# Optimization experiments

Measured on AMD Instinct MI355X. Metric: run time of the kernel, lower is better.

The kernel has to match this reference:

```python
import jax, jax.numpy as jnp
import numpy as np

B, S, D = 64, 512, 768
H1, H2, NC = 256, 128, 1
THR = 0.1  # attention_threshold in original forward


def setup_inputs() -> dict:
    key = jax.random.key(0)
    k0, k1, k2, k3 = jax.random.split(key, 4)
    # scale hidden states so H @ H^T logits are in a reasonable softmax range
    hidden_states = jax.random.normal(k0, (B, S, D), jnp.float32) * 0.05
    attention_mask = jnp.ones((B, S), jnp.int32)
    W1 = jax.random.normal(k1, (D, H1), jnp.float32) * (1.0 / np.sqrt(D))
    b1 = jnp.zeros((H1,), jnp.float32)
    W2 = jax.random.normal(k2, (H1, H2), jnp.float32) * (1.0 / np.sqrt(H1))
    b2 = jnp.zeros((H2,), jnp.float32)
    Wc = jax.random.normal(k3, (H2, NC), jnp.float32) * (1.0 / np.sqrt(H2))
    bc = jnp.zeros((NC,), jnp.float32)
    return dict(hidden_states=hidden_states, attention_mask=attention_mask,
                W1=W1, b1=b1, W2=W2, b2=b2, Wc=Wc, bc=bc)


def _gcn_adj(att):
    # thresholded sparse graph, expressed as masked dense adjacency [B,S,S]
    A = jnp.where(att > THR, att, 0.0)
    # PyG add_remaining_self_loops: keep existing self-loop weight, else fill 1.0
    diag = jnp.diagonal(att, axis1=-2, axis2=-1)            # [B,S]
    diag = jnp.where(diag > THR, diag, 1.0)
    i = jnp.arange(att.shape[-1])
    A = A.at[:, i, i].set(diag)
    # gcn_norm: deg over targets (columns), D^{-1/2} A D^{-1/2}
    deg = A.sum(axis=-2)                                     # [B,S]
    dis = jnp.where(deg > 0, jax.lax.rsqrt(deg), 0.0)
    return dis[:, :, None] * A * dis[:, None, :]


def _gcn_layer(Ahat, x, W, b):
    xw = x @ W                                               # linear first (no bias)
    # out[target j] = sum_source i  Ahat[i,j] * xw[i]
    return jnp.einsum('bij,bih->bjh', Ahat, xw) + b


def reference(hidden_states, attention_mask, W1, b1, W2, b2, Wc, bc):
    att = jax.nn.softmax(
        jnp.einsum('bsd,btd->bst', hidden_states, hidden_states), axis=-1)
    Ahat = _gcn_adj(att)                                     # [B,S,S]
    x = jax.nn.relu(_gcn_layer(Ahat, hidden_states, W1, b1))  # dropout inactive (eval)
    x = _gcn_layer(Ahat, x, W2, b2)                          # [B,S,H2]
    m = attention_mask.astype(x.dtype)                       # masked mean over valid tokens
    emb = (x * m[:, :, None]).sum(axis=1) / m.sum(axis=1, keepdims=True)
    return jax.nn.sigmoid(emb @ Wc + bc)                     # [B,1]
```

## Files before the change

kernel.cpp:

```cpp
#include <hip/hip_runtime.h>
#include <hip/hip_bf16.h>
#include <math.h>

constexpr int B = 64, S = 512, D = 768, H1 = 256, H2 = 128;
constexpr float THR = 0.1f;

typedef short bf16x8 __attribute__((ext_vector_type(8)));
typedef float f32x4 __attribute__((ext_vector_type(4)));
typedef unsigned int uint_t;
typedef const __attribute__((address_space(1))) unsigned int* gptr_t;
typedef __attribute__((address_space(3))) unsigned int* lptr_t;

__device__ __forceinline__ unsigned short f2bf(float f) {
    unsigned int u = __builtin_bit_cast(unsigned int, f);
    unsigned int r = (u + 0x7FFFu + ((u >> 16) & 1u)) >> 16;
    return (unsigned short)r;
}
__device__ __forceinline__ float bf2f(unsigned short b) {
    return __builtin_bit_cast(float, (unsigned int)b << 16);
}
__device__ __forceinline__ unsigned char f2fp8(float f) {
    uint_t u = __builtin_bit_cast(uint_t, f);
    u += 0x7FFFFu + ((u >> 20) & 1u);
    return (unsigned char)((((u >> 23) - 120u) << 3) | ((u >> 20) & 7u));
}
__device__ __forceinline__ float fp82f(unsigned char q) {
    uint_t e = (q >> 3) & 0xFu, m = q & 7u;
    if (e == 0) return (float)m * 0.001953125f;
    return __builtin_bit_cast(float, ((e + 120u) << 23) | (m << 20));
}
__device__ __forceinline__ void gl2lds16(const void* g, void* l) {
    __builtin_amdgcn_global_load_lds((gptr_t)g, (lptr_t)l, 16, 0, 0);
}

__global__ __launch_bounds__(256) void k_cast(const float* __restrict__ in,
                                              short* __restrict__ out,
                                              const float* __restrict__ W1,
                                              short* __restrict__ W1T,
                                              const float* __restrict__ W2,
                                              short* __restrict__ W2T,
                                              float* __restrict__ zbuf) {
    const int id = blockIdx.x * 256 + threadIdx.x;
    if (id < 18432) ((float4*)zbuf)[id] = make_float4(0.f, 0.f, 0.f, 0.f);
    if (id < 196608) {
        const int n = id / D, k = id - n * D;
        W1T[id] = (short)f2bf(W1[(size_t)k * H1 + n]);
    } else if (id < 229376) {
        const int i2 = id - 196608;
        const int n = i2 / H1, k = i2 - n * H1;
        W2T[i2] = (short)f2bf(W2[(size_t)k * H2 + n]);
    }
    for (int i = id; i < 3145728; i += 524288) {
        float4 a = ((const float4*)in)[i * 2];
        float4 b = ((const float4*)in)[i * 2 + 1];
        uint4 o;
        o.x = (uint_t)f2bf(a.x) | ((uint_t)f2bf(a.y) << 16);
        o.y = (uint_t)f2bf(a.z) | ((uint_t)f2bf(a.w) << 16);
        o.z = (uint_t)f2bf(b.x) | ((uint_t)f2bf(b.y) << 16);
        o.w = (uint_t)f2bf(b.z) | ((uint_t)f2bf(b.w) << 16);
        ((uint4*)out)[i] = o;
    }
}

__global__ __launch_bounds__(256) void k_logits(const short* __restrict__ Hb_,
                                                unsigned char* __restrict__ L8,
                                                float* __restrict__ rsum) {
    const int orig = blockIdx.x;
    const int wg = (orig & 7) * 128 + (orig >> 3);
    const int bz = wg >> 4;
    const int bi = (wg >> 2) & 3, bj = wg & 3;
    const short* Ab = Hb_ + (size_t)bz * S * D;
    unsigned char* Lb = L8 + (size_t)bz * S * S;
    float* rs = rsum + bz * S;
    const int M0 = bi * 128, N0 = bj * 128;

    __shared__ __align__(16) short As[8192];
    __shared__ __align__(16) short Bs[8192];

    const int tid = threadIdx.x, lane = tid & 63, wid = tid >> 6;
    const int wm = (wid & 1) * 64, wn = (wid >> 1) * 64;
    const int r_in = lane >> 3, kc = lane & 7;
    const int kswz = ((kc ^ r_in) << 3);

    f32x4 zero = {0.f, 0.f, 0.f, 0.f};
    f32x4 acc[4][4];
    #pragma unroll
    for (int mi = 0; mi < 4; ++mi)
        #pragma unroll
        for (int nj = 0; nj < 4; ++nj) acc[mi][nj] = zero;

    for (int t = 0; t < 12; ++t) {
        const int kt = t * 64;
        #pragma unroll
        for (int q = 0; q < 4; ++q) {
            const int ch = wid * 4 + q;
            gl2lds16(Ab + (size_t)(M0 + ch * 8 + r_in) * D + kt + kswz, &As[ch * 512]);
        }
        #pragma unroll
        for (int q = 0; q < 4; ++q) {
            const int ch = wid * 4 + q;
            gl2lds16(Ab + (size_t)(N0 + ch * 8 + r_in) * D + kt + kswz, &Bs[ch * 512]);
        }
        __syncthreads();
        #pragma unroll
        for (int kk = 0; kk < 2; ++kk) {
            bf16x8 af[4], bfr[4];
            const int g0 = kk * 4 + (lane >> 4);
            #pragma unroll
            for (int mi = 0; mi < 4; ++mi) {
                const int row = wm + mi * 16 + (lane & 15);
                af[mi] = *(const bf16x8*)&As[row * 64 + ((g0 ^ (row & 7)) << 3)];
            }
            #pragma unroll
            for (int nj = 0; nj < 4; ++nj) {
                const int row = wn + nj * 16 + (lane & 15);
                bfr[nj] = *(const bf16x8*)&Bs[row * 64 + ((g0 ^ (row & 7)) << 3)];
            }
            #pragma unroll
            for (int mi = 0; mi < 4; ++mi)
                #pragma unroll
                for (int nj = 0; nj < 4; ++nj)
                    acc[mi][nj] = __builtin_amdgcn_mfma_f32_16x16x32_bf16(
                        af[mi], bfr[nj], acc[mi][nj], 0, 0, 0);
        }
        __syncthreads();
    }

    #pragma unroll
    for (int mi = 0; mi < 4; ++mi)
        #pragma unroll
        for (int nj = 0; nj < 4; ++nj) {
            f32x4 v = acc[mi][nj];
            acc[mi][nj][0] = __expf(v[0]);
            acc[mi][nj][1] = __expf(v[1]);
            acc[mi][nj][2] = __expf(v[2]);
            acc[mi][nj][3] = __expf(v[3]);
        }

    #pragma unroll
    for (int mi = 0; mi < 4; ++mi) {
        const int mb = wm + mi * 16 + (lane >> 4) * 4;
        #pragma unroll
        for (int nj = 0; nj < 4; ++nj) {
            const int n = wn + nj * 16 + (lane & 15);
            f32x4 v = acc[mi][nj];
            uchar4 o;
            o.x = f2fp8(v[0]); o.y = f2fp8(v[1]);
            o.z = f2fp8(v[2]); o.w = f2fp8(v[3]);
            *(uchar4*)&Lb[(size_t)(N0 + n) * S + M0 + mb] = o;
        }
    }

    #pragma unroll
    for (int mi = 0; mi < 4; ++mi)
        #pragma unroll
        for (int r = 0; r < 4; ++r) {
            float s = acc[mi][0][r] + acc[mi][1][r] + acc[mi][2][r] + acc[mi][3][r];
            s += __shfl_xor(s, 1); s += __shfl_xor(s, 2);
            s += __shfl_xor(s, 4); s += __shfl_xor(s, 8);
            if ((lane & 15) == 0)
                atomicAdd(&rs[M0 + wm + mi * 16 + (lane >> 4) * 4 + r], s);
        }
}

__global__ __launch_bounds__(256) void k_prep_gemm(
    const unsigned char* __restrict__ L8, const float* __restrict__ rsum,
    const int* __restrict__ mask, float* __restrict__ dis,
    float* __restrict__ wacc, uint_t* __restrict__ ents, uint_t* __restrict__ cnts,
    const short* __restrict__ W1T, const short* __restrict__ Hb,
    short* __restrict__ xw1) {
    __shared__ __align__(16) short As[128 * 64];
    __shared__ __align__(16) short Bs[64 * 64];

    const int blk = blockIdx.x;
    const int r9 = blk % 9;
    const int tid = threadIdx.x, lane = tid & 63, wid = tid >> 6;

    if (r9 != 8) {
        const int p = (blk / 9) * 8 + r9;
        const int j = p * 4 + (tid >> 6);
        const int b = j >> 9, jl = j & (S - 1);
        const size_t base = (size_t)b * S * S + (size_t)jl * S + lane * 8;
        const uint2 r = *(const uint2*)(L8 + base);
        const int i0 = lane * 8;
        const float4 sa = *(const float4*)&rsum[b * S + i0];
        const float4 sb = *(const float4*)&rsum[b * S + i0 + 4];
        const float rsv[8] = {sa.x, sa.y, sa.z, sa.w, sb.x, sb.y, sb.z, sb.w};
        float a[8];
        float deg = 0.f;
        #pragma unroll
        for (int e = 0; e < 8; ++e) {
            const unsigned char q = (e < 4) ? (unsigned char)(r.x >> (e * 8))
                                            : (unsigned char)(r.y >> ((e - 4) * 8));
            float att = fp82f(q) / rsv[e];
            if (i0 + e == jl) a[e] = (att > THR) ? att : 1.0f;
            else              a[e] = (att > THR) ? att : 0.0f;
            deg += a[e];
        }
        #pragma unroll
        for (int off = 1; off < 64; off <<= 1) deg += __shfl_xor(deg, off);
        const float d = (deg > 0.f) ? rsqrtf(deg) : 0.f;
        const float cv = d * (float)mask[j];
        if (lane == 0) dis[j] = d;
        #pragma unroll
        for (int e = 0; e < 8; ++e)
            if (a[e] != 0.f) atomicAdd(&wacc[b * S + i0 + e], cv * a[e]);

        unsigned long long bl[8];
        #pragma unroll
        for (int e = 0; e < 8; ++e) bl[e] = __ballot(a[e] != 0.f);
        const unsigned long long lt = (lane == 0) ? 0ull : (~0ull >> (64 - lane));
        int pre = 0, tot = 0;
        #pragma unroll
        for (int e = 0; e < 8; ++e) {
            pre += __popcll(bl[e] & lt);
            tot += __popcll(bl[e]);
        }
        uint_t* rowents = ents + (size_t)j * S;
        int own = 0;
        #pragma unroll
        for (int e = 0; e < 8; ++e) {
            if (a[e] != 0.f) {
                rowents[pre + own] = ((uint_t)(i0 + e) << 16) | (uint_t)f2bf(a[e]);
                ++own;
            }
        }
        if (lane == 0) cnts[j] = (uint_t)tot;
        return;
    }

    const int orig = blk / 9;
    const int wg = (orig & 7) * 128 + (orig >> 3);
    const int bx = wg & 1, by = wg >> 1;
    const int M0 = bx * 128, N0 = by * 64;

    const int wm = (wid & 1) * 64, wn = (wid >> 1) * 32;
    const int r_in = lane >> 3, kc = lane & 7;
    const int kswz = ((kc ^ r_in) << 3);

    f32x4 zero = {0.f, 0.f, 0.f, 0.f};
    f32x4 acc[4][2];
    #pragma unroll
    for (int mi = 0; mi < 4; ++mi) {
        acc[mi][0] = zero; acc[mi][1] = zero;
    }

    for (int t = 0; t < 12; ++t) {
        const int kt = t << 6;
        #pragma unroll
        for (int q = 0; q < 4; ++q) {
            const int ch = wid * 4 + q;
            gl2lds16(W1T + (size_t)(M0 + ch * 8 + r_in) * D + kt + kswz, &As[ch * 512]);
        }
        #pragma unroll
        for (int q = 0; q < 2; ++q) {
            const int ch = wid * 2 + q;
            gl2lds16(Hb + (size_t)(N0 + ch * 8 + r_in) * D + kt + kswz, &Bs[ch * 512]);
        }
        __syncthreads();
        #pragma unroll
        for (int kk = 0; kk < 2; ++kk) {
            bf16x8 af[4], bfr[2];
            const int g0 = kk * 4 + (lane >> 4);
            #pragma unroll
            for (int mi = 0; mi < 4; ++mi) {
                const int row = wm + mi * 16 + (lane & 15);
                af[mi] = *(const bf16x8*)&As[row * 64 + ((g0 ^ (row & 7)) << 3)];
            }
            #pragma unroll
            for (int nj = 0; nj < 2; ++nj) {
                const int row = wn + nj * 16 + (lane & 15);
                bfr[nj] = *(const bf16x8*)&Bs[row * 64 + ((g0 ^ (row & 7)) << 3)];
            }
            #pragma unroll
            for (int mi = 0; mi < 4; ++mi)
                #pragma unroll
                for (int nj = 0; nj < 2; ++nj)
                    acc[mi][nj] = __builtin_amdgcn_mfma_f32_16x16x32_bf16(
                        af[mi], bfr[nj], acc[mi][nj], 0, 0, 0);
        }
        __syncthreads();
    }

    #pragma unroll
    for (int mi = 0; mi < 4; ++mi) {
        const int m = M0 + wm + mi * 16 + (lane >> 4) * 4;
        #pragma unroll
        for (int nj = 0; nj < 2; ++nj) {
            const int n = N0 + wn + nj * 16 + (lane & 15);
            f32x4 v = acc[mi][nj];
            ushort4 o = make_ushort4(f2bf(v[0]), f2bf(v[1]), f2bf(v[2]), f2bf(v[3]));
            *(ushort4*)&xw1[(size_t)n * H1 + m] = o;
        }
    }
}

__global__ __launch_bounds__(256) void k_agg(const uint_t* __restrict__ ents,
                                             const uint_t* __restrict__ cnts,
                                             const float* __restrict__ dis,
                                             const short* __restrict__ xw1,
                                             const float* __restrict__ b1,
                                             short* __restrict__ y1) {
    const int tid = threadIdx.x;
    const int h = tid;
    const float bias = b1[h];
    __shared__ uint_t sents[S];
    for (int jj = 0; jj < 8; ++jj) {
        const int j = blockIdx.x * 8 + jj;
        const int b = j >> 9;
        const int cnt = (int)cnts[j];
        for (int k = tid; k < cnt; k += 256) sents[k] = ents[(size_t)j * S + k];
        __syncthreads();
        float acc = 0.f;
        for (int k = 0; k < cnt; ++k) {
            const uint_t p = sents[k];
            const int i = (int)(p >> 16);
            const float val = bf2f((unsigned short)(p & 0xFFFFu)) * dis[b * S + i];
            acc += val * bf2f((unsigned short)xw1[(size_t)(b * S + i) * H1 + h]);
        }
        const float o = fmaxf(dis[j] * acc + bias, 0.f);
        y1[(size_t)j * H1 + h] = (short)f2bf(o);
        __syncthreads();
    }
}

__global__ __launch_bounds__(256) void k_gemm_emb(
    const short* __restrict__ W2T, const short* __restrict__ y1,
    const float* __restrict__ wacc, const float* __restrict__ dis,
    float* __restrict__ embp) {
    const int orig = blockIdx.x;
    const int wg = (orig & 7) * 64 + (orig >> 3);
    const int N0 = wg * 64;

    __shared__ __align__(16) short As[128 * 64];
    __shared__ __align__(16) short Bs[64 * 64];

    const int tid = threadIdx.x, lane = tid & 63, wid = tid >> 6;
    const int wm = (wid & 1) * 64, wn = (wid >> 1) * 32;
    const int r_in = lane >> 3, kc = lane & 7;
    const int kswz = ((kc ^ r_in) << 3);

    f32x4 zero = {0.f, 0.f, 0.f, 0.f};
    f32x4 acc[4][2];
    #pragma unroll
    for (int mi = 0; mi < 4; ++mi) {
        acc[mi][0] = zero; acc[mi][1] = zero;
    }

    for (int t = 0; t < 4; ++t) {
        const int kt = t << 6;
        #pragma unroll
        for (int q = 0; q < 4; ++q) {
            const int ch = wid * 4 + q;
            gl2lds16(W2T + (size_t)(ch * 8 + r_in) * H1 + kt + kswz, &As[ch * 512]);
        }
        #pragma unroll
        for (int q = 0; q < 2; ++q) {
            const int ch = wid * 2 + q;
            gl2lds16(y1 + (size_t)(N0 + ch * 8 + r_in) * H1 + kt + kswz, &Bs[ch * 512]);
        }
        __syncthreads();
        #pragma unroll
        for (int kk = 0; kk < 2; ++kk) {
            bf16x8 af[4], bfr[2];
            const int g0 = kk * 4 + (lane >> 4);
            #pragma unroll
            for (int mi = 0; mi < 4; ++mi) {
                const int row = wm + mi * 16 + (lane & 15);
                af[mi] = *(const bf16x8*)&As[row * 64 + ((g0 ^ (row & 7)) << 3)];
            }
            #pragma unroll
            for (int nj = 0; nj < 2; ++nj) {
                const int row = wn + nj * 16 + (lane & 15);
                bfr[nj] = *(const bf16x8*)&Bs[row * 64 + ((g0 ^ (row & 7)) << 3)];
            }
            #pragma unroll
            for (int mi = 0; mi < 4; ++mi)
                #pragma unroll
                for (int nj = 0; nj < 2; ++nj)
                    acc[mi][nj] = __builtin_amdgcn_mfma_f32_16x16x32_bf16(
                        af[mi], bfr[nj], acc[mi][nj], 0, 0, 0);
        }
        __syncthreads();
    }

    const int bb = N0 >> 9;
    float wv[2];
    #pragma unroll
    for (int nj = 0; nj < 2; ++nj) {
        const int gn = N0 + wn + nj * 16 + (lane & 15);
        wv[nj] = wacc[gn] * dis[gn];
    }
    #pragma unroll
    for (int mi = 0; mi < 4; ++mi)
        #pragma unroll
        for (int r = 0; r < 4; ++r) {
            float s = acc[mi][0][r] * wv[0] + acc[mi][1][r] * wv[1];
            s += __shfl_xor(s, 1); s += __shfl_xor(s, 2);
            s += __shfl_xor(s, 4); s += __shfl_xor(s, 8);
            if ((lane & 15) == 0) {
                const int h = wm + mi * 16 + (lane >> 4) * 4 + r;
                atomicAdd(&embp[bb * H2 + h], s);
            }
        }
}

__global__ __launch_bounds__(128) void k_final(const float* __restrict__ emb,
                                               const int* __restrict__ mask,
                                               const float* __restrict__ b2,
                                               const float* __restrict__ Wc,
                                               const float* __restrict__ bc,
                                               float* __restrict__ out) {
    const int b = blockIdx.x;
    const int h = threadIdx.x;
    const int* mb = mask + b * S;

    float msum = 0.f;
    for (int i = h; i < S; i += 128) msum += (float)mb[i];
    #pragma unroll
    for (int off = 1; off < 64; off <<= 1) msum += __shfl_xor(msum, off);
    __shared__ float redm[2], redv[2];
    if ((h & 63) == 0) redm[h >> 6] = msum;
    __syncthreads();
    msum = redm[0] + redm[1];

    const float e = b2[h] + emb[b * H2 + h] / msum;
    float val = e * Wc[h];
    #pragma unroll
    for (int off = 1; off < 64; off <<= 1) val += __shfl_xor(val, off);
    if ((h & 63) == 0) redv[h >> 6] = val;
    __syncthreads();
    if (h == 0) {
        float z = redv[0] + redv[1] + bc[0];
        out[b] = 1.f / (1.f + expf(-z));
    }
}

extern "C" void kernel_launch(void* const* d_in, const int* in_sizes, int n_in,
                              void* d_out, int out_size, void* d_ws, size_t ws_size,
                              hipStream_t stream) {
    const float* H    = (const float*)d_in[0];
    const int*   mask = (const int*)d_in[1];
    const float* W1   = (const float*)d_in[2];
    const float* b1   = (const float*)d_in[3];
    const float* W2   = (const float*)d_in[4];
    const float* b2   = (const float*)d_in[5];
    const float* Wc   = (const float*)d_in[6];
    const float* bc   = (const float*)d_in[7];
    float* out = (float*)d_out;

    const int NTOK = B * S;

    char* wsb = (char*)d_ws;
    short* Hb    = (short*)(wsb);
    short* y1    = (short*)(wsb);
    unsigned char* Lbuf = (unsigned char*)(wsb + 50331648);
    short* xw1   = (short*)(wsb + 83886080);
    float* rsum  = (float*)(wsb + 109051904);
    float* wacc  = rsum + NTOK;
    float* emb   = wacc + NTOK;
    float* dis   = emb + 8192;
    short* W1T   = (short*)(dis + NTOK);
    short* W2T   = W1T + 196608;
    uint_t* ents = (uint_t*)(wsb + 134217728);
    uint_t* cnts = (uint_t*)(wsb + 201326592);

    k_cast<<<2048, 256, 0, stream>>>(H, Hb, W1, W1T, W2, W2T, rsum);

    k_logits<<<1024, 256, 0, stream>>>(Hb, Lbuf, rsum);

    k_prep_gemm<<<9216, 256, 0, stream>>>(Lbuf, rsum, mask, dis, wacc, ents, cnts,
                                          W1T, Hb, xw1);

    k_agg<<<4096, 256, 0, stream>>>(ents, cnts, dis, xw1, b1, y1);

    k_gemm_emb<<<512, 256, 0, stream>>>(W2T, y1, wacc, dis, emb);

    k_final<<<B, 128, 0, stream>>>(emb, mask, b2, Wc, bc, out);
}
```

Measured before the change: 142.7 us.

## Fuse fp32-to-bf16 cast of hidden states into logits GEMM tile loads

The separate pass that converted the full hidden-state tensor to bf16 is removed. The logits kernel now reads fp32 directly, converts it in registers and stores into LDS. Diagonal tiles also write the bf16 copy to global memory for later kernels, and they reuse the A tile as the B operand. This removes a full read and write of the hidden states and one launch. In exchange the logits kernel does twice the global load bytes through plain synchronous loads instead of async global-to-LDS loads, which exposes more load latency.

Measured after the change: 151.5 us. +6.2%, slower.

```diff
diff --git a/kernel.cpp b/kernel.cpp
--- a/kernel.cpp
+++ b/kernel.cpp
@@ -32,10 +32,16 @@
 __device__ __forceinline__ void gl2lds16(const void* g, void* l) {
     __builtin_amdgcn_global_load_lds((gptr_t)g, (lptr_t)l, 16, 0, 0);
 }
-
-__global__ __launch_bounds__(256) void k_cast(const float* __restrict__ in,
-                                              short* __restrict__ out,
-                                              const float* __restrict__ W1,
+__device__ __forceinline__ uint4 pack8(const float4& a, const float4& b) {
+    uint4 o;
+    o.x = (uint_t)f2bf(a.x) | ((uint_t)f2bf(a.y) << 16);
+    o.y = (uint_t)f2bf(a.z) | ((uint_t)f2bf(a.w) << 16);
+    o.z = (uint_t)f2bf(b.x) | ((uint_t)f2bf(b.y) << 16);
+    o.w = (uint_t)f2bf(b.z) | ((uint_t)f2bf(b.w) << 16);
+    return o;
+}
+
+__global__ __launch_bounds__(256) void k_cast(const float* __restrict__ W1,
                                               short* __restrict__ W1T,
                                               const float* __restrict__ W2,
                                               short* __restrict__ W2T,
@@ -50,26 +56,19 @@
         const int n = i2 / H1, k = i2 - n * H1;
         W2T[i2] = (short)f2bf(W2[(size_t)k * H2 + n]);
     }
-    for (int i = id; i < 3145728; i += 524288) {
-        float4 a = ((const float4*)in)[i * 2];
-        float4 b = ((const float4*)in)[i * 2 + 1];
-        uint4 o;
-        o.x = (uint_t)f2bf(a.x) | ((uint_t)f2bf(a.y) << 16);
-        o.y = (uint_t)f2bf(a.z) | ((uint_t)f2bf(a.w) << 16);
-        o.z = (uint_t)f2bf(b.x) | ((uint_t)f2bf(b.y) << 16);
-        o.w = (uint_t)f2bf(b.z) | ((uint_t)f2bf(b.w) << 16);
-        ((uint4*)out)[i] = o;
-    }
-}
-
-__global__ __launch_bounds__(256) void k_logits(const short* __restrict__ Hb_,
+}
+
+__global__ __launch_bounds__(256) void k_logits(const float* __restrict__ H,
+                                                short* __restrict__ HbW,
                                                 unsigned char* __restrict__ L8,
                                                 float* __restrict__ rsum) {
     const int orig = blockIdx.x;
     const int wg = (orig & 7) * 128 + (orig >> 3);
     const int bz = wg >> 4;
     const int bi = (wg >> 2) & 3, bj = wg & 3;
-    const short* Ab = Hb_ + (size_t)bz * S * D;
+    const bool diag = (bi == bj);
+    const float* Hf = H + (size_t)bz * S * D;
+    short* Hw = HbW + (size_t)bz * S * D;
     unsigned char* Lb = L8 + (size_t)bz * S * S;
     float* rs = rsum + bz * S;
     const int M0 = bi * 128, N0 = bj * 128;
@@ -80,7 +79,6 @@
     const int tid = threadIdx.x, lane = tid & 63, wid = tid >> 6;
     const int wm = (wid & 1) * 64, wn = (wid >> 1) * 64;
     const int r_in = lane >> 3, kc = lane & 7;
-    const int kswz = ((kc ^ r_in) << 3);
 
     f32x4 zero = {0.f, 0.f, 0.f, 0.f};
     f32x4 acc[4][4];
@@ -89,17 +87,29 @@
         #pragma unroll
         for (int nj = 0; nj < 4; ++nj) acc[mi][nj] = zero;
 
+    const short* Bsrc = diag ? As : Bs;
+
     for (int t = 0; t < 12; ++t) {
-        const int kt = t * 64;
+        const int col = t * 64 + ((kc ^ r_in) << 3);
         #pragma unroll
         for (int q = 0; q < 4; ++q) {
             const int ch = wid * 4 + q;
-            gl2lds16(Ab + (size_t)(M0 + ch * 8 + r_in) * D + kt + kswz, &As[ch * 512]);
-        }
-        #pragma unroll
-        for (int q = 0; q < 4; ++q) {
-            const int ch = wid * 4 + q;
-            gl2lds16(Ab + (size_t)(N0 + ch * 8 + r_in) * D + kt + kswz, &Bs[ch * 512]);
+            const int row = M0 + ch * 8 + r_in;
+            const float4 a = *(const float4*)&Hf[(size_t)row * D + col];
+            const float4 b = *(const float4*)&Hf[(size_t)row * D + col + 4];
+            const uint4 o = pack8(a, b);
+            *(uint4*)&As[ch * 512 + lane * 8] = o;
+            if (diag) *(uint4*)&Hw[(size_t)row * D + col] = o;
+        }
+        if (!diag) {
+            #pragma unroll
+            for (int q = 0; q < 4; ++q) {
+                const int ch = wid * 4 + q;
+                const int row = N0 + ch * 8 + r_in;
+                const float4 a = *(const float4*)&Hf[(size_t)row * D + col];
+                const float4 b = *(const float4*)&Hf[(size_t)row * D + col + 4];
+                *(uint4*)&Bs[ch * 512 + lane * 8] = pack8(a, b);
+            }
         }
         __syncthreads();
         #pragma unroll
@@ -114,7 +124,7 @@
             #pragma unroll
             for (int nj = 0; nj < 4; ++nj) {
                 const int row = wn + nj * 16 + (lane & 15);
-                bfr[nj] = *(const bf16x8*)&Bs[row * 64 + ((g0 ^ (row & 7)) << 3)];
+                bfr[nj] = *(const bf16x8*)&Bsrc[row * 64 + ((g0 ^ (row & 7)) << 3)];
             }
             #pragma unroll
             for (int mi = 0; mi < 4; ++mi)
@@ -465,9 +475,9 @@
     uint_t* ents = (uint_t*)(wsb + 134217728);
     uint_t* cnts = (uint_t*)(wsb + 201326592);
 
-    k_cast<<<2048, 256, 0, stream>>>(H, Hb, W1, W1T, W2, W2T, rsum);
-
-    k_logits<<<1024, 256, 0, stream>>>(Hb, Lbuf, rsum);
+    k_cast<<<1024, 256, 0, stream>>>(W1, W1T, W2, W2T, rsum);
+
+    k_logits<<<1024, 256, 0, stream>>>(H, Hb, Lbuf, rsum);
 
     k_prep_gemm<<<9216, 256, 0, stream>>>(Lbuf, rsum, mask, dis, wacc, ents, cnts,
                                           W1T, Hb, xw1);
```

## Fuse sparse layer-1 aggregation into layer-2 GEMM with y1 kept in LDS

Applied to the files above, without the earlier changes.

Merges the sparse aggregation kernel into the second GEMM/embedding kernel: each 64-token block first computes its relu'd layer-1 outputs into padded shared memory, then feeds them directly as the B operand of the MFMA GEMM. It also changes aggregation from one token per 256-thread block to one token per wavefront, with each lane covering four features and edges broadcast by shuffle instead of LDS plus syncthreads. This drops the y1 global round-trip and a kernel launch, but the grid falls from 4096 to 512 blocks, so the irregular aggregation has less parallelism and may be bound by latency.

New measurement: 145.2 us. Within noise of the previous version (+1.7%).

```diff
diff --git a/kernel.cpp b/kernel.cpp
--- a/kernel.cpp
+++ b/kernel.cpp
@@ -295,47 +295,49 @@
     }
 }
 
-__global__ __launch_bounds__(256) void k_agg(const uint_t* __restrict__ ents,
-                                             const uint_t* __restrict__ cnts,
-                                             const float* __restrict__ dis,
-                                             const short* __restrict__ xw1,
-                                             const float* __restrict__ b1,
-                                             short* __restrict__ y1) {
-    const int tid = threadIdx.x;
-    const int h = tid;
-    const float bias = b1[h];
-    __shared__ uint_t sents[S];
-    for (int jj = 0; jj < 8; ++jj) {
-        const int j = blockIdx.x * 8 + jj;
-        const int b = j >> 9;
-        const int cnt = (int)cnts[j];
-        for (int k = tid; k < cnt; k += 256) sents[k] = ents[(size_t)j * S + k];
-        __syncthreads();
-        float acc = 0.f;
-        for (int k = 0; k < cnt; ++k) {
-            const uint_t p = sents[k];
-            const int i = (int)(p >> 16);
-            const float val = bf2f((unsigned short)(p & 0xFFFFu)) * dis[b * S + i];
-            acc += val * bf2f((unsigned short)xw1[(size_t)(b * S + i) * H1 + h]);
-        }
-        const float o = fmaxf(dis[j] * acc + bias, 0.f);
-        y1[(size_t)j * H1 + h] = (short)f2bf(o);
-        __syncthreads();
-    }
-}
-
-__global__ __launch_bounds__(256) void k_gemm_emb(
-    const short* __restrict__ W2T, const short* __restrict__ y1,
-    const float* __restrict__ wacc, const float* __restrict__ dis,
-    float* __restrict__ embp) {
+__global__ __launch_bounds__(256) void k_agg_emb(
+    const uint_t* __restrict__ ents, const uint_t* __restrict__ cnts,
+    const float* __restrict__ dis, const float* __restrict__ wacc,
+    const short* __restrict__ xw1, const float* __restrict__ b1,
+    const short* __restrict__ W2T, float* __restrict__ embp) {
+    constexpr int YP = 264;
+    __shared__ __align__(16) short y1s[64 * YP];
+    __shared__ __align__(16) short As[128 * 64];
+
     const int orig = blockIdx.x;
     const int wg = (orig & 7) * 64 + (orig >> 3);
     const int N0 = wg * 64;
-
-    __shared__ __align__(16) short As[128 * 64];
-    __shared__ __align__(16) short Bs[64 * 64];
-
+    const int b = N0 >> 9;
     const int tid = threadIdx.x, lane = tid & 63, wid = tid >> 6;
+
+    for (int u = 0; u < 16; ++u) {
+        const int jj = wid * 16 + u;
+        const int j = N0 + jj;
+        const int cnt = (int)cnts[j];
+        float acc0 = 0.f, acc1 = 0.f, acc2 = 0.f, acc3 = 0.f;
+        for (int k0 = 0; k0 < cnt; k0 += 64) {
+            uint_t my = 0;
+            if (k0 + lane < cnt) my = ents[(size_t)j * S + k0 + lane];
+            const int lim = (cnt - k0 < 64) ? (cnt - k0) : 64;
+            for (int k = 0; k < lim; ++k) {
+                const uint_t p = __shfl(my, k);
+                const int i = (int)(p >> 16);
+                const float val = bf2f((unsigned short)(p & 0xFFFFu)) * dis[b * S + i];
+                const short* xr = &xw1[(size_t)(b * S + i) * H1];
+                acc0 += val * bf2f((unsigned short)xr[lane]);
+                acc1 += val * bf2f((unsigned short)xr[lane + 64]);
+                acc2 += val * bf2f((unsigned short)xr[lane + 128]);
+                acc3 += val * bf2f((unsigned short)xr[lane + 192]);
+            }
+        }
+        const float dj = dis[j];
+        y1s[jj * YP + lane      ] = (short)f2bf(fmaxf(dj * acc0 + b1[lane      ], 0.f));
+        y1s[jj * YP + lane + 64 ] = (short)f2bf(fmaxf(dj * acc1 + b1[lane + 64 ], 0.f));
+        y1s[jj * YP + lane + 128] = (short)f2bf(fmaxf(dj * acc2 + b1[lane + 128], 0.f));
+        y1s[jj * YP + lane + 192] = (short)f2bf(fmaxf(dj * acc3 + b1[lane + 192], 0.f));
+    }
+    __syncthreads();
+
     const int wm = (wid & 1) * 64, wn = (wid >> 1) * 32;
     const int r_in = lane >> 3, kc = lane & 7;
     const int kswz = ((kc ^ r_in) << 3);
@@ -354,11 +356,6 @@
             const int ch = wid * 4 + q;
             gl2lds16(W2T + (size_t)(ch * 8 + r_in) * H1 + kt + kswz, &As[ch * 512]);
         }
-        #pragma unroll
-        for (int q = 0; q < 2; ++q) {
-            const int ch = wid * 2 + q;
-            gl2lds16(y1 + (size_t)(N0 + ch * 8 + r_in) * H1 + kt + kswz, &Bs[ch * 512]);
-        }
         __syncthreads();
         #pragma unroll
         for (int kk = 0; kk < 2; ++kk) {
@@ -371,8 +368,9 @@
             }
             #pragma unroll
             for (int nj = 0; nj < 2; ++nj) {
-                const int row = wn + nj * 16 + (lane & 15);
-                bfr[nj] = *(const bf16x8*)&Bs[row * 64 + ((g0 ^ (row & 7)) << 3)];
+                const int tok = wn + nj * 16 + (lane & 15);
+                const int col = kt + kk * 32 + (lane >> 4) * 8;
+                bfr[nj] = *(const bf16x8*)&y1s[tok * YP + col];
             }
             #pragma unroll
             for (int mi = 0; mi < 4; ++mi)
@@ -384,7 +382,6 @@
         __syncthreads();
     }
 
-    const int bb = N0 >> 9;
     float wv[2];
     #pragma unroll
     for (int nj = 0; nj < 2; ++nj) {
@@ -400,7 +397,7 @@
             s += __shfl_xor(s, 4); s += __shfl_xor(s, 8);
             if ((lane & 15) == 0) {
                 const int h = wm + mi * 16 + (lane >> 4) * 4 + r;
-                atomicAdd(&embp[bb * H2 + h], s);
+                atomicAdd(&embp[b * H2 + h], s);
             }
         }
 }
@@ -453,7 +450,6 @@
 
     char* wsb = (char*)d_ws;
     short* Hb    = (short*)(wsb);
-    short* y1    = (short*)(wsb);
     unsigned char* Lbuf = (unsigned char*)(wsb + 50331648);
     short* xw1   = (short*)(wsb + 83886080);
     float* rsum  = (float*)(wsb + 109051904);
@@ -472,9 +468,7 @@
     k_prep_gemm<<<9216, 256, 0, stream>>>(Lbuf, rsum, mask, dis, wacc, ents, cnts,
                                           W1T, Hb, xw1);
 
-    k_agg<<<4096, 256, 0, stream>>>(ents, cnts, dis, xw1, b1, y1);
-
-    k_gemm_emb<<<512, 256, 0, stream>>>(W2T, y1, wacc, dis, emb);
+    k_agg_emb<<<512, 256, 0, stream>>>(ents, cnts, dis, wacc, xw1, b1, W2T, emb);
 
     k_final<<<B, 128, 0, stream>>>(emb, mask, b2, Wc, bc, out);
 }
```
